# Performance work log

Measured on AMD Instinct MI355X. Metric: run time of the kernel, lower is better.

The kernel has to match this reference:

```python
import jax, jax.numpy as jnp
import numpy as np

B, K, T, C = 4, 8, 2048, 64

def setup_inputs() -> dict:
    key = jax.random.key(0)
    ks = jax.random.split(key, 7)
    return {
        "x": jax.random.normal(ks[0], (B, K, T, C), dtype=jnp.float32),
        "Wq": jax.random.normal(ks[1], (C, C), dtype=jnp.float32) / np.sqrt(C),
        "bq": jax.random.normal(ks[2], (C,), dtype=jnp.float32) * 0.01,
        "Wk": jax.random.normal(ks[3], (C, C), dtype=jnp.float32) / np.sqrt(C),
        "bk": jax.random.normal(ks[4], (C,), dtype=jnp.float32) * 0.01,
        "Wv": jax.random.normal(ks[5], (C, C), dtype=jnp.float32) / np.sqrt(C),
        "bv": jax.random.normal(ks[6], (C,), dtype=jnp.float32) * 0.01,
    }

def reference(x, Wq, bq, Wk, bk, Wv, bv):
    c_dim = x.shape[-1]
    # torch nn.Linear: y = x @ W.T + b
    q = jnp.einsum('bktc,dc->bktd', x, Wq) + bq
    k = jnp.einsum('bktc,dc->bktd', x, Wk) + bk
    v = jnp.einsum('bktc,dc->bktd', x, Wv) + bv
    scores = jnp.einsum('bkic,bkjc->bkij', q, k) / jnp.sqrt(jnp.float32(c_dim))
    attn = jax.nn.softmax(scores, axis=-1)
    out = jnp.einsum('bkij,bkjc->bkic', attn, v)
    return out
```

## Files before the change

kernel.cpp:

```cpp
#include <hip/hip_runtime.h>


#define T_DIM 2048
#define NHEAD 32
#define HSTRIDE (T_DIM * 64)
#define QSCALE 0.18033688011112042f
#define SOFF  8.0f

#define SWZ(row, grp) ((row) * 64 + ((((grp) ^ ((row) & 7)) & 7) * 8))

typedef _Float16 h8 __attribute__((ext_vector_type(8)));
typedef _Float16 h4 __attribute__((ext_vector_type(4)));
typedef __fp16   g2 __attribute__((ext_vector_type(2)));
typedef float    f4 __attribute__((ext_vector_type(4)));
typedef float    fv16 __attribute__((ext_vector_type(16)));

union H4U { h4 v; g2 p[2]; };
union H8U { h8 v; h4 h[2]; g2 p[4]; };

#if defined(__has_builtin)
#if __has_builtin(__builtin_amdgcn_exp2f)
#define EXP2(x) __builtin_amdgcn_exp2f(x)
#endif
#endif
#ifndef EXP2
__device__ inline float exp2_raw(float x) {
    float r;
    asm("v_exp_f32 %0, %1" : "=v"(r) : "v"(x));
    return r;
}
#define EXP2(x) exp2_raw(x)
#endif

__device__ inline h4 cvt4(f4 x) {
    H4U u;
    u.p[0] = __builtin_amdgcn_cvt_pkrtz(x[0], x[1]);
    u.p[1] = __builtin_amdgcn_cvt_pkrtz(x[2], x[3]);
    return u.v;
}

__device__ inline h8 cvt8(f4 a, f4 b) {
    H8U r;
    r.h[0] = cvt4(a);
    r.h[1] = cvt4(b);
    return r.v;
}

__device__ inline fv16 splat16(float x) {
    fv16 r;
    #pragma unroll
    for (int i = 0; i < 16; ++i) r[i] = x;
    return r;
}

__global__ __launch_bounds__(256) void qkv_proj_kernel(
    const float* __restrict__ x,
    const float* __restrict__ Wq, const float* __restrict__ bq,
    const float* __restrict__ Wk, const float* __restrict__ bk,
    const float* __restrict__ Wv, const float* __restrict__ bv,
    _Float16* __restrict__ qh, _Float16* __restrict__ khT,
    _Float16* __restrict__ vtT)
{
    __shared__ _Float16 ws[3][64 * 64];
    __shared__ float bsh[3][64];

    const int tid  = threadIdx.x;
    const int row0 = blockIdx.x * 64;
    const int head = blockIdx.x >> 5;
    const int t0   = (blockIdx.x & 31) * 64;

    const int w    = tid >> 6;
    const int lane = tid & 63;
    const int l15  = lane & 15;
    const int qd   = lane >> 4;

    f4 xa[2][2];
    {
        const float* xp = x + (size_t)(row0 + w * 16 + l15) * 64 + qd * 8;
        #pragma unroll
        for (int ch = 0; ch < 2; ++ch) {
            xa[ch][0] = *(const f4*)(xp + ch * 32);
            xa[ch][1] = *(const f4*)(xp + ch * 32 + 4);
        }
    }

    #pragma unroll
    for (int m = 0; m < 3; ++m) {
        const float* Wm = (m == 0) ? Wq : ((m == 1) ? Wk : Wv);
        const float* bm = (m == 0) ? bq : ((m == 1) ? bk : bv);
        #pragma unroll
        for (int pass = 0; pass < 4; ++pass) {
            const int idx = pass * 1024 + tid * 4;
            const int d = idx >> 6, c = idx & 63;
            f4 wv = *(const f4*)(Wm + idx);
            *(h4*)&ws[m][SWZ(d, c >> 3) + (c & 7)] = cvt4(wv);
        }
        if (tid < 64) bsh[m][tid] = bm[tid];
    }

    h8 af[2];
    #pragma unroll
    for (int ch = 0; ch < 2; ++ch)
        af[ch] = cvt8(xa[ch][0], xa[ch][1]);

    __syncthreads();

    f4 acc[3][4];
    #pragma unroll
    for (int m = 0; m < 3; ++m) {
        h8 bf[4][2];
        #pragma unroll
        for (int ns = 0; ns < 4; ++ns)
            #pragma unroll
            for (int ch = 0; ch < 2; ++ch)
                bf[ns][ch] = *(const h8*)&ws[m][SWZ(ns * 16 + l15, ch * 4 + qd)];
        #pragma unroll
        for (int ns = 0; ns < 4; ++ns)
            acc[m][ns] = (f4){0.f, 0.f, 0.f, 0.f};
        #pragma unroll
        for (int ch = 0; ch < 2; ++ch)
            #pragma unroll
            for (int ns = 0; ns < 4; ++ns)
                acc[m][ns] = __builtin_amdgcn_mfma_f32_16x16x32_f16(
                    af[ch], bf[ns][ch], acc[m][ns], 0, 0, 0);
    }

    __syncthreads();

    #pragma unroll
    for (int m = 0; m < 2; ++m) {
        #pragma unroll
        for (int ns = 0; ns < 4; ++ns) {
            const int d = ns * 16 + l15;
            const float bias = bsh[m][d];
            #pragma unroll
            for (int r = 0; r < 4; ++r) {
                const int t = w * 16 + qd * 4 + r;
                float v = acc[m][ns][r] + bias;
                if (m == 0) v *= QSCALE;
                ws[m][SWZ(t, d >> 3) + (d & 7)] = (_Float16)v;
            }
        }
    }
    #pragma unroll
    for (int ns = 0; ns < 4; ++ns) {
        const int d = ns * 16 + l15;
        const float bias = bsh[2][d];
        const int tl = w * 16 + qd * 4;
        f4 pvf;
        #pragma unroll
        for (int r = 0; r < 4; ++r)
            pvf[r] = acc[2][ns][r] + bias;
        *(h4*)&ws[2][SWZ(d, tl >> 3) + (tl & 7)] = cvt4(pvf);
    }

    __syncthreads();

    #pragma unroll
    for (int pass = 0; pass < 2; ++pass) {
        const int t  = pass * 32 + (tid >> 3);
        const int c0 = (tid & 7) * 8;
        *(h8*)&qh[(size_t)(row0 + t) * 64 + c0] =
            *(const h8*)&ws[0][SWZ(t, tid & 7)];
    }
    #pragma unroll
    for (int pass = 0; pass < 2; ++pass) {
        const int f   = pass * 2048 + tid * 8;
        const int kb  = f >> 11;
        const int cs  = (f >> 9) & 3;
        const int l   = (f >> 3) & 63;
        const int p   = l & 31;
        const int w16 = p & 15;
        const int sw  = ((w16 & 12) == 4) ? (w16 + 4)
                      : (((w16 & 12) == 8) ? (w16 - 4) : w16);
        const int tact = kb * 32 + (p & 16) + sw;
        const int g8   = cs * 2 + (l >> 5);
        *(h8*)&khT[(size_t)head * HSTRIDE + (t0 >> 6) * 4096 + f] =
            *(const h8*)&ws[1][SWZ(tact, g8)];
    }
    #pragma unroll
    for (int pass = 0; pass < 2; ++pass) {
        const int f  = pass * 2048 + tid * 8;
        const int q2 = f >> 9;
        const int b  = q2 >> 1, cc = q2 & 1;
        const int l  = (f >> 3) & 63;
        const int c  = cc * 32 + (l & 31);
        const int tg = b * 2 + (l >> 5);
        *(h8*)&vtT[(size_t)head * HSTRIDE + (t0 >> 6) * 4096 + f] =
            *(const h8*)&ws[2][SWZ(c, tg)];
    }
}

__global__ __launch_bounds__(256, 2) void attn_kernel(
    const _Float16* __restrict__ qh, const _Float16* __restrict__ khT,
    const _Float16* __restrict__ vtT, float* __restrict__ out)
{
    __shared__ float xbuf[2][4224];

    const int tid  = threadIdx.x;
    const int w    = tid >> 6;
    const int lane = tid & 63;
    const int l31  = lane & 31;
    const int lh   = lane >> 5;

    const int bid  = blockIdx.x;
    const int xcd  = bid & 7;
    const int idx  = bid >> 3;
    const int head = xcd * 4 + (idx >> 5);
    const int qchunk = idx & 31;
    const int q0   = qchunk * 64;

    h8 qf[2][4];
    #pragma unroll
    for (int qs = 0; qs < 2; ++qs) {
        const _Float16* qp = qh + (size_t)(head * T_DIM + q0 + qs * 32 + l31) * 64 + lh * 8;
        #pragma unroll
        for (int cs = 0; cs < 4; ++cs)
            qf[qs][cs] = *(const h8*)(qp + cs * 16);
    }

    const int ko = lane * 8;
    const _Float16* kbase = khT + (size_t)head * HSTRIDE + (size_t)w * 8 * 4096;
    const _Float16* vbase = vtT + (size_t)head * HSTRIDE + (size_t)w * 8 * 4096;

    f4 rs4[2] = {(f4){0.f,0.f,0.f,0.f}, (f4){0.f,0.f,0.f,0.f}};
    fv16 oacc[2][2];
    #pragma unroll
    for (int qs = 0; qs < 2; ++qs)
        #pragma unroll
        for (int cc = 0; cc < 2; ++cc)
            oacc[qs][cc] = splat16(0.f);

    h8 kf[2][4];
    h8 vf[4][2];
    #pragma unroll
    for (int kb = 0; kb < 2; ++kb)
        #pragma unroll
        for (int cs = 0; cs < 4; ++cs)
            kf[kb][cs] = *(const h8*)(kbase + kb * 2048 + cs * 512 + ko);
    #pragma unroll
    for (int b = 0; b < 4; ++b)
        #pragma unroll
        for (int cc = 0; cc < 2; ++cc)
            vf[b][cc] = *(const h8*)(vbase + (b * 2 + cc) * 512 + ko);

    for (int it = 0; it < 8; ++it) {
        const _Float16* kn = kbase + (size_t)(it + 1) * 4096;
        const _Float16* vn = vbase + (size_t)(it + 1) * 4096;
        const bool more = (it < 7);

        #pragma unroll
        for (int kb = 0; kb < 2; ++kb) {
            fv16 st2[2];
            st2[0] = splat16(-SOFF);
            st2[1] = splat16(-SOFF);
            #pragma unroll
            for (int cs = 0; cs < 4; ++cs)
                #pragma unroll
                for (int qs = 0; qs < 2; ++qs)
                    st2[qs] = __builtin_amdgcn_mfma_f32_32x32x16_f16(
                        kf[kb][cs], qf[qs][cs], st2[qs], 0, 0, 0);

            if (more) {
                #pragma unroll
                for (int cs = 0; cs < 4; ++cs)
                    kf[kb][cs] = *(const h8*)(kn + kb * 2048 + cs * 512 + ko);
            }

            #pragma unroll
            for (int qs = 0; qs < 2; ++qs) {
                f4 pg[4];
                #pragma unroll
                for (int g = 0; g < 4; ++g) {
                    pg[g][0] = EXP2(st2[qs][4 * g + 0]);
                    pg[g][1] = EXP2(st2[qs][4 * g + 1]);
                    pg[g][2] = EXP2(st2[qs][4 * g + 2]);
                    pg[g][3] = EXP2(st2[qs][4 * g + 3]);
                    rs4[qs] += pg[g];
                }
                H8U pa[2];
                #pragma unroll
                for (int g = 0; g < 4; ++g) {
                    pa[g >> 1].p[(g & 1) * 2 + 0] = __builtin_amdgcn_cvt_pkrtz(pg[g][0], pg[g][1]);
                    pa[g >> 1].p[(g & 1) * 2 + 1] = __builtin_amdgcn_cvt_pkrtz(pg[g][2], pg[g][3]);
                }
                #pragma unroll
                for (int bl = 0; bl < 2; ++bl)
                    #pragma unroll
                    for (int cc = 0; cc < 2; ++cc)
                        oacc[qs][cc] = __builtin_amdgcn_mfma_f32_32x32x16_f16(
                            pa[bl].v, vf[kb * 2 + bl][cc], oacc[qs][cc], 0, 0, 0);
            }

            if (more) {
                #pragma unroll
                for (int bl = 0; bl < 2; ++bl)
                    #pragma unroll
                    for (int cc = 0; cc < 2; ++cc)
                        vf[kb * 2 + bl][cc] =
                            *(const h8*)(vn + ((kb * 2 + bl) * 2 + cc) * 512 + ko);
            }
        }
    }

    float ls0, ls1;
    {
        float a = (rs4[0][0] + rs4[0][1]) + (rs4[0][2] + rs4[0][3]);
        a += __shfl_xor(a, 32, 64);
        ls0 = a;
        float b = (rs4[1][0] + rs4[1][1]) + (rs4[1][2] + rs4[1][3]);
        b += __shfl_xor(b, 32, 64);
        ls1 = b;
    }

    if (w >= 2) {
        float* xb = xbuf[w - 2];
        #pragma unroll
        for (int qs = 0; qs < 2; ++qs)
            #pragma unroll
            for (int cc = 0; cc < 2; ++cc)
                #pragma unroll
                for (int r = 0; r < 16; ++r)
                    xb[(qs * 2 + cc) * 1024 + r * 64 + lane] = oacc[qs][cc][r];
        xb[4096 + lane] = ls0;
        xb[4160 + lane] = ls1;
    }
    __syncthreads();
    if (w < 2) {
        const float* xb = xbuf[w];
        #pragma unroll
        for (int qs = 0; qs < 2; ++qs)
            #pragma unroll
            for (int cc = 0; cc < 2; ++cc)
                #pragma unroll
                for (int r = 0; r < 16; ++r)
                    oacc[qs][cc][r] += xb[(qs * 2 + cc) * 1024 + r * 64 + lane];
        ls0 += xb[4096 + lane];
        ls1 += xb[4160 + lane];
    }
    __syncthreads();

    if (w == 0) {
        float* xb = xbuf[1];
        #pragma unroll
        for (int cc = 0; cc < 2; ++cc)
            #pragma unroll
            for (int r = 0; r < 16; ++r)
                xb[(2 + cc) * 1024 + r * 64 + lane] = oacc[1][cc][r];
        xb[4160 + lane] = ls1;
    } else if (w == 1) {
        float* xb = xbuf[0];
        #pragma unroll
        for (int cc = 0; cc < 2; ++cc)
            #pragma unroll
            for (int r = 0; r < 16; ++r)
                xb[cc * 1024 + r * 64 + lane] = oacc[0][cc][r];
        xb[4096 + lane] = ls0;
    }
    __syncthreads();

    if (w == 0) {
        const float* xb = xbuf[0];
        fv16 of[2];
        #pragma unroll
        for (int cc = 0; cc < 2; ++cc)
            #pragma unroll
            for (int r = 0; r < 16; ++r)
                of[cc][r] = oacc[0][cc][r] + xb[cc * 1024 + r * 64 + lane];
        const float lt = ls0 + xb[4096 + lane];
        const float linv = 1.f / lt;
        #pragma unroll
        for (int r = 0; r < 16; ++r) {
            const int qrow = (r & 3) + 8 * (r >> 2) + 4 * lh;
            const float fac = __shfl(linv, qrow, 64);
            #pragma unroll
            for (int cc = 0; cc < 2; ++cc)
                out[(size_t)(head * T_DIM + q0 + qrow) * 64 + cc * 32 + l31] =
                    of[cc][r] * fac;
        }
    } else if (w == 1) {
        const float* xb = xbuf[1];
        fv16 of[2];
        #pragma unroll
        for (int cc = 0; cc < 2; ++cc)
            #pragma unroll
            for (int r = 0; r < 16; ++r)
                of[cc][r] = oacc[1][cc][r] + xb[(2 + cc) * 1024 + r * 64 + lane];
        const float lt = ls1 + xb[4160 + lane];
        const float linv = 1.f / lt;
        #pragma unroll
        for (int r = 0; r < 16; ++r) {
            const int qrow = (r & 3) + 8 * (r >> 2) + 4 * lh;
            const float fac = __shfl(linv, qrow, 64);
            #pragma unroll
            for (int cc = 0; cc < 2; ++cc)
                out[(size_t)(head * T_DIM + q0 + 32 + qrow) * 64 + cc * 32 + l31] =
                    of[cc][r] * fac;
        }
    }
}

extern "C" void kernel_launch(void* const* d_in, const int* in_sizes, int n_in,
                              void* d_out, int out_size, void* d_ws, size_t ws_size,
                              hipStream_t stream)
{
    (void)in_sizes; (void)n_in; (void)out_size; (void)ws_size;
    const float* x  = (const float*)d_in[0];
    const float* Wq = (const float*)d_in[1];
    const float* bq = (const float*)d_in[2];
    const float* Wk = (const float*)d_in[3];
    const float* bk = (const float*)d_in[4];
    const float* Wv = (const float*)d_in[5];
    const float* bv = (const float*)d_in[6];
    float* out = (float*)d_out;

    _Float16* qh  = (_Float16*)d_ws;
    _Float16* khT = qh + (size_t)NHEAD * HSTRIDE;
    _Float16* vtT = khT + (size_t)NHEAD * HSTRIDE;

    hipLaunchKernelGGL(qkv_proj_kernel, dim3(1024), dim3(256), 0, stream,
                       x, Wq, bq, Wk, bk, Wv, bv, qh, khT, vtT);
    hipLaunchKernelGGL(attn_kernel, dim3(1024), dim3(256), 0, stream,
                       qh, khT, vtT, out);
}
```

Measured before the change: 124.9 us.

## Load projection weights directly into registers and raise priority around attention MFMAs

The QKV projection kernel no longer stages the weight matrices and biases through shared memory. Each lane loads its weight fragments and bias values straight from global memory and converts them to fp16 in registers, which removes one __syncthreads and the LDS round trip. In exchange, weight loads are replicated across the four waves and are less coalesced. Separately, the attention kernel wraps its MFMA and softmax sections in s_setprio(1)/s_setprio(0) so that waves in compute phases get issue priority over waves that are issuing loads.

```diff
diff --git a/kernel.cpp b/kernel.cpp
--- a/kernel.cpp
+++ b/kernel.cpp
@@ -61,8 +61,7 @@
     _Float16* __restrict__ qh, _Float16* __restrict__ khT,
     _Float16* __restrict__ vtT)
 {
-    __shared__ _Float16 ws[3][64 * 64];
-    __shared__ float bsh[3][64];
+    __shared__ _Float16 ot[3][64 * 64];
 
     const int tid  = threadIdx.x;
     const int row0 = blockIdx.x * 64;
@@ -84,36 +83,31 @@
         }
     }
 
+    float bb[3][4];
+    #pragma unroll
+    for (int ns = 0; ns < 4; ++ns) {
+        bb[0][ns] = bq[ns * 16 + l15];
+        bb[1][ns] = bk[ns * 16 + l15];
+        bb[2][ns] = bv[ns * 16 + l15];
+    }
+
+    h8 af[2];
+    #pragma unroll
+    for (int ch = 0; ch < 2; ++ch)
+        af[ch] = cvt8(xa[ch][0], xa[ch][1]);
+
+    f4 acc[3][4];
     #pragma unroll
     for (int m = 0; m < 3; ++m) {
         const float* Wm = (m == 0) ? Wq : ((m == 1) ? Wk : Wv);
-        const float* bm = (m == 0) ? bq : ((m == 1) ? bk : bv);
-        #pragma unroll
-        for (int pass = 0; pass < 4; ++pass) {
-            const int idx = pass * 1024 + tid * 4;
-            const int d = idx >> 6, c = idx & 63;
-            f4 wv = *(const f4*)(Wm + idx);
-            *(h4*)&ws[m][SWZ(d, c >> 3) + (c & 7)] = cvt4(wv);
-        }
-        if (tid < 64) bsh[m][tid] = bm[tid];
-    }
-
-    h8 af[2];
-    #pragma unroll
-    for (int ch = 0; ch < 2; ++ch)
-        af[ch] = cvt8(xa[ch][0], xa[ch][1]);
-
-    __syncthreads();
-
-    f4 acc[3][4];
-    #pragma unroll
-    for (int m = 0; m < 3; ++m) {
         h8 bf[4][2];
         #pragma unroll
         for (int ns = 0; ns < 4; ++ns)
             #pragma unroll
-            for (int ch = 0; ch < 2; ++ch)
-                bf[ns][ch] = *(const h8*)&ws[m][SWZ(ns * 16 + l15, ch * 4 + qd)];
+            for (int ch = 0; ch < 2; ++ch) {
+                const float* wp = Wm + (ns * 16 + l15) * 64 + ch * 32 + qd * 8;
+                bf[ns][ch] = cvt8(*(const f4*)wp, *(const f4*)(wp + 4));
+            }
         #pragma unroll
         for (int ns = 0; ns < 4; ++ns)
             acc[m][ns] = (f4){0.f, 0.f, 0.f, 0.f};
@@ -125,33 +119,31 @@
                     af[ch], bf[ns][ch], acc[m][ns], 0, 0, 0);
     }
 
-    __syncthreads();
-
     #pragma unroll
     for (int m = 0; m < 2; ++m) {
         #pragma unroll
         for (int ns = 0; ns < 4; ++ns) {
             const int d = ns * 16 + l15;
-            const float bias = bsh[m][d];
+            const float bias = bb[m][ns];
             #pragma unroll
             for (int r = 0; r < 4; ++r) {
                 const int t = w * 16 + qd * 4 + r;
                 float v = acc[m][ns][r] + bias;
                 if (m == 0) v *= QSCALE;
-                ws[m][SWZ(t, d >> 3) + (d & 7)] = (_Float16)v;
+                ot[m][SWZ(t, d >> 3) + (d & 7)] = (_Float16)v;
             }
         }
     }
     #pragma unroll
     for (int ns = 0; ns < 4; ++ns) {
         const int d = ns * 16 + l15;
-        const float bias = bsh[2][d];
+        const float bias = bb[2][ns];
         const int tl = w * 16 + qd * 4;
         f4 pvf;
         #pragma unroll
         for (int r = 0; r < 4; ++r)
             pvf[r] = acc[2][ns][r] + bias;
-        *(h4*)&ws[2][SWZ(d, tl >> 3) + (tl & 7)] = cvt4(pvf);
+        *(h4*)&ot[2][SWZ(d, tl >> 3) + (tl & 7)] = cvt4(pvf);
     }
 
     __syncthreads();
@@ -161,7 +153,7 @@
         const int t  = pass * 32 + (tid >> 3);
         const int c0 = (tid & 7) * 8;
         *(h8*)&qh[(size_t)(row0 + t) * 64 + c0] =
-            *(const h8*)&ws[0][SWZ(t, tid & 7)];
+            *(const h8*)&ot[0][SWZ(t, tid & 7)];
     }
     #pragma unroll
     for (int pass = 0; pass < 2; ++pass) {
@@ -176,7 +168,7 @@
         const int tact = kb * 32 + (p & 16) + sw;
         const int g8   = cs * 2 + (l >> 5);
         *(h8*)&khT[(size_t)head * HSTRIDE + (t0 >> 6) * 4096 + f] =
-            *(const h8*)&ws[1][SWZ(tact, g8)];
+            *(const h8*)&ot[1][SWZ(tact, g8)];
     }
     #pragma unroll
     for (int pass = 0; pass < 2; ++pass) {
@@ -187,7 +179,7 @@
         const int c  = cc * 32 + (l & 31);
         const int tg = b * 2 + (l >> 5);
         *(h8*)&vtT[(size_t)head * HSTRIDE + (t0 >> 6) * 4096 + f] =
-            *(const h8*)&ws[2][SWZ(c, tg)];
+            *(const h8*)&ot[2][SWZ(c, tg)];
     }
 }
 
@@ -251,6 +243,7 @@
 
         #pragma unroll
         for (int kb = 0; kb < 2; ++kb) {
+            __builtin_amdgcn_s_setprio(1);
             fv16 st2[2];
             st2[0] = splat16(-SOFF);
             st2[1] = splat16(-SOFF);
@@ -260,6 +253,7 @@
                 for (int qs = 0; qs < 2; ++qs)
                     st2[qs] = __builtin_amdgcn_mfma_f32_32x32x16_f16(
                         kf[kb][cs], qf[qs][cs], st2[qs], 0, 0, 0);
+            __builtin_amdgcn_s_setprio(0);
 
             if (more) {
                 #pragma unroll
@@ -267,6 +261,7 @@
                     kf[kb][cs] = *(const h8*)(kn + kb * 2048 + cs * 512 + ko);
             }
 
+            __builtin_amdgcn_s_setprio(1);
             #pragma unroll
             for (int qs = 0; qs < 2; ++qs) {
                 f4 pg[4];
@@ -291,6 +286,7 @@
                         oacc[qs][cc] = __builtin_amdgcn_mfma_f32_32x32x16_f16(
                             pa[bl].v, vf[kb * 2 + bl][cc], oacc[qs][cc], 0, 0, 0);
             }
+            __builtin_amdgcn_s_setprio(0);
 
             if (more) {
                 #pragma unroll
```

New measurement: 144.4 us. 1.16x slower.
